# Optimization experiments

Hardware: AMD Instinct MI355X
Metric: run time of the kernel (lower is better)

Reference implementation:

```python
import jax, jax.numpy as jnp
import numpy as np

# ---------- helpers ----------

def _sqdist(a, b):
    # a: (B,n,3), b: (B,m,3) -> squared distances (B,n,m)
    return (jnp.sum(a * a, -1)[..., :, None] + jnp.sum(b * b, -1)[..., None, :]
            - 2.0 * jnp.einsum('bnd,bmd->bnm', a, b))

_gather = jax.vmap(lambda pts, idx: pts[idx])  # (N,C),(S,K)->(S,K,C) over batch


def _fps(xyz, npoint):
    # farthest point sampling; indices are non-differentiable (as in CUDA op)
    xyz = jax.lax.stop_gradient(xyz)
    B, N, _ = xyz.shape
    mind0 = jnp.sum((xyz - xyz[:, :1]) ** 2, -1)  # dist to point 0

    def step(mind, _):
        idx = jnp.argmax(mind, -1)                       # (B,)
        nxt = jnp.take_along_axis(xyz, idx[:, None, None], 1)  # (B,1,3)
        mind = jnp.minimum(mind, jnp.sum((xyz - nxt) ** 2, -1))
        return mind, idx.astype(jnp.int32)

    _, idxs = jax.lax.scan(step, mind0, None, length=npoint - 1)
    return jnp.concatenate([jnp.zeros((B, 1), jnp.int32), idxs.T], 1)  # (B,npoint)


def _ball_query(xyz, new_xyz, radius, nsample):
    # first nsample points within radius of each center, pad with first hit
    d2 = jax.lax.stop_gradient(_sqdist(new_xyz, xyz))  # (B,S,N)
    N = xyz.shape[1]
    mask = d2 < radius * radius
    key = jnp.where(mask, 0, N) + jnp.arange(N, dtype=jnp.int32)  # in-ball first, original order
    order = jnp.argsort(key, -1)
    idx = order[..., :nsample]
    cnt = mask.sum(-1, keepdims=True)
    return jnp.where(jnp.arange(nsample) < cnt, idx, idx[..., :1])


def _mlp(x, params):
    # shared MLP: 1x1 conv (+BN folded: default eval stats -> affine bias) + ReLU
    for W, b in params:
        x = jax.nn.relu(jnp.einsum('...c,co->...o', x, W) + b)
    return x


def _sa(xyz, feats, npoint, radius, nsample, params):
    # PointnetSAModuleVotes: FPS + ball-query + group(use_xyz, normalize_xyz) + MLP + max-pool
    inds = _fps(xyz, npoint)
    new_xyz = _gather(xyz, inds)                              # (B,S,3)
    idx = _ball_query(xyz, new_xyz, radius, nsample)          # (B,S,K)
    g = (_gather(xyz, idx) - new_xyz[:, :, None, :]) / radius  # normalize_xyz
    if feats is not None:
        g = jnp.concatenate([g, _gather(feats, idx)], -1)     # use_xyz: xyz first
    g = _mlp(g, params)
    return new_xyz, jnp.max(g, 2), inds                       # max over nsample


def _fp(unknown, known, feats1, feats2, params):
    # PointnetFPModule: 3-NN inverse-(squared)distance interpolation + MLP
    d2 = jax.lax.stop_gradient(_sqdist(unknown, known))       # (B,n,m)
    negd, idx = jax.lax.top_k(-d2, 3)
    d = jnp.maximum(-negd, 0.0)
    w = 1.0 / (d + 1e-8)
    w = w / jnp.sum(w, -1, keepdims=True)                     # (B,n,3)
    interp = jnp.sum(w[..., None] * _gather(feats2, idx), 2)  # (B,n,C2)
    return _mlp(jnp.concatenate([feats1, interp], -1), params)


_SPECS = {
    'sa1': [(3, 32), (32, 32), (32, 64)],
    'sa2': [(67, 64), (64, 128)],
    'sa3': [(131, 128), (128, 256)],
    'sa4': [(259, 256), (256, 256)],
    'fp1': [(512, 256), (256, 128)],
    'fp2': [(256, 128), (128, 64)],
}


def setup_inputs() -> dict:
    key = jax.random.key(0)
    ks = iter(jax.random.split(key, 64))
    inp = {'pointcloud': jax.random.uniform(next(ks), (4, 32768, 3), jnp.float32)}
    for name, dims in _SPECS.items():
        for i, (ci, co) in enumerate(dims):
            inp[f'{name}_w{i}'] = jax.random.normal(next(ks), (ci, co), jnp.float32) * 0.02
            inp[f'{name}_b{i}'] = jnp.zeros((co,), jnp.float32)
    return inp


def reference(pointcloud,
              sa1_w0, sa1_b0, sa1_w1, sa1_b1, sa1_w2, sa1_b2,
              sa2_w0, sa2_b0, sa2_w1, sa2_b1,
              sa3_w0, sa3_b0, sa3_w1, sa3_b1,
              sa4_w0, sa4_b0, sa4_w1, sa4_b1,
              fp1_w0, fp1_b0, fp1_w1, fp1_b1,
              fp2_w0, fp2_b0, fp2_w1, fp2_b1):
    P = {
        'sa1': [(sa1_w0, sa1_b0), (sa1_w1, sa1_b1), (sa1_w2, sa1_b2)],
        'sa2': [(sa2_w0, sa2_b0), (sa2_w1, sa2_b1)],
        'sa3': [(sa3_w0, sa3_b0), (sa3_w1, sa3_b1)],
        'sa4': [(sa4_w0, sa4_b0), (sa4_w1, sa4_b1)],
        'fp1': [(fp1_w0, fp1_b0), (fp1_w1, fp1_b1)],
        'fp2': [(fp2_w0, fp2_b0), (fp2_w1, fp2_b1)],
    }
    xyz = pointcloud[..., :3]  # input_feature_dim = 0 -> no extra features
    xyz1, f1, _ = _sa(xyz, None, 512, 0.1, 64, P['sa1'])
    xyz2, f2, _ = _sa(xyz1, f1, 256, 0.2, 32, P['sa2'])
    xyz3, f3, _ = _sa(xyz2, f2, 64, 0.4, 16, P['sa3'])
    xyz4, f4, _ = _sa(xyz3, f3, 16, 0.8, 16, P['sa4'])
    f = _fp(xyz3, xyz4, f3, f4, P['fp1'])   # (B,64,128)
    f = _fp(xyz2, xyz3, f2, f, P['fp2'])    # (B,256,64) == torch feats.transpose(1,2)
    return f, xyz2
```

## Files before the change

### kernel.cpp

```cpp
#include <hip/hip_runtime.h>
#include <cstddef>


__device__ __forceinline__ float sqd(float x, float y, float z, float qx, float qy, float qz) {
#pragma clang fp contract(off)
    float dx = x - qx, dy = y - qy, dz = z - qz;
    return (dx * dx + dy * dy) + dz * dz;
}

__device__ __forceinline__ float sum3sq(float x, float y, float z) {
#pragma clang fp contract(off)
    return (x * x + y * y) + z * z;
}

__device__ __forceinline__ float sqd_dot(float ax, float ay, float az, float sa_,
                                         float bx, float by, float bz) {
#pragma clang fp contract(off)
    float sb = (bx * bx + by * by) + bz * bz;
    float dt = (ax * bx + ay * by) + az * bz;
    return (sa_ + sb) - 2.0f * dt;
}

__device__ __forceinline__ unsigned long long packkey(float v, int orig) {
    return ((unsigned long long)__float_as_uint(v) << 32) | (unsigned)(~orig);
}


__global__ __launch_bounds__(512) void fps_sub(const float* __restrict__ xyz,
                                               int* __restrict__ inds,
                                               float4* __restrict__ SPall) {
    const int b = blockIdx.x, t = threadIdx.x, w = t >> 6, l = t & 63;
    const float* __restrict__ P = xyz + (size_t)b * 32768 * 3;
    float4* __restrict__ SP = SPall + (size_t)b * 32768;

    __shared__ float mind[32768];
    __shared__ int   cntS[512], offS[512], curS[512];
    __shared__ unsigned long long bkeyS[512];
    __shared__ float bxS[512], byS[512], bzS[512];
    __shared__ unsigned long long candK[8];
    __shared__ int   candB[8];
    __shared__ float bbS[6];
    __shared__ float scr[48];
    __shared__ int   qcntS;

    float mnx = 1e30f, mny = 1e30f, mnz = 1e30f;
    float mxx = -1e30f, mxy = -1e30f, mxz = -1e30f;
    for (int p = t; p < 32768; p += 512) {
        const float x = P[3 * p], y = P[3 * p + 1], z = P[3 * p + 2];
        mnx = fminf(mnx, x); mxx = fmaxf(mxx, x);
        mny = fminf(mny, y); mxy = fmaxf(mxy, y);
        mnz = fminf(mnz, z); mxz = fmaxf(mxz, z);
    }
#pragma unroll
    for (int o = 1; o < 64; o <<= 1) {
        mnx = fminf(mnx, __shfl_xor(mnx, o)); mxx = fmaxf(mxx, __shfl_xor(mxx, o));
        mny = fminf(mny, __shfl_xor(mny, o)); mxy = fmaxf(mxy, __shfl_xor(mxy, o));
        mnz = fminf(mnz, __shfl_xor(mnz, o)); mxz = fmaxf(mxz, __shfl_xor(mxz, o));
    }
    if (l == 0) {
        scr[w] = mnx; scr[8 + w] = mny; scr[16 + w] = mnz;
        scr[24 + w] = mxx; scr[32 + w] = mxy; scr[40 + w] = mxz;
    }
    __syncthreads();
    if (t == 0) {
        float a0 = 1e30f, a1 = 1e30f, a2 = 1e30f, a3 = -1e30f, a4 = -1e30f, a5 = -1e30f;
        for (int i = 0; i < 8; ++i) {
            a0 = fminf(a0, scr[i]);      a1 = fminf(a1, scr[8 + i]);
            a2 = fminf(a2, scr[16 + i]); a3 = fmaxf(a3, scr[24 + i]);
            a4 = fmaxf(a4, scr[32 + i]); a5 = fmaxf(a5, scr[40 + i]);
        }
        bbS[0] = a0; bbS[1] = a1; bbS[2] = a2; bbS[3] = a3; bbS[4] = a4; bbS[5] = a5;
        qcntS = 0;
    }
    __syncthreads();
    const float bx0 = bbS[0], by0 = bbS[1], bz0 = bbS[2];
    const float ex = bbS[3] - bx0, ey = bbS[4] - by0, ez = bbS[5] - bz0;
    const float ivx = ex > 1e-20f ? 8.0f / ex : 0.0f;
    const float ivy = ey > 1e-20f ? 8.0f / ey : 0.0f;
    const float ivz = ez > 1e-20f ? 8.0f / ez : 0.0f;

    cntS[t] = 0;
    __syncthreads();
    for (int p = t; p < 32768; p += 512) {
        const float x = P[3 * p], y = P[3 * p + 1], z = P[3 * p + 2];
        const int ix = min(7, (int)((x - bx0) * ivx));
        const int iy = min(7, (int)((y - by0) * ivy));
        const int iz = min(7, (int)((z - bz0) * ivz));
        atomicAdd(&cntS[(iz * 8 + iy) * 8 + ix], 1);
    }
    __syncthreads();

    offS[t] = cntS[t];
    __syncthreads();
    for (int d = 1; d < 512; d <<= 1) {
        const int v = (t >= d) ? offS[t - d] : 0;
        __syncthreads();
        offS[t] += v;
        __syncthreads();
    }
    const int myexc = offS[t] - cntS[t];
    offS[t] = myexc;
    curS[t] = myexc;
    __syncthreads();

    for (int p = t; p < 32768; p += 512) {
        const float x = P[3 * p], y = P[3 * p + 1], z = P[3 * p + 2];
        const int ix = min(7, (int)((x - bx0) * ivx));
        const int iy = min(7, (int)((y - by0) * ivy));
        const int iz = min(7, (int)((z - bz0) * ivz));
        const int pos = atomicAdd(&curS[(iz * 8 + iy) * 8 + ix], 1);
        SP[pos] = make_float4(x, y, z, __int_as_float(p));
    }
    for (int s = t; s < 32768; s += 512) mind[s] = 1e30f;
    const int myCnt = cntS[t];
    bkeyS[t] = (myCnt > 0) ? packkey(1e30f, 0x7fffffff) : 0ull;
    bxS[t] = 0.f; byS[t] = 0.f; bzS[t] = 0.f;
    if (t == 0) inds[b * 512] = 0;

    const int oix = t & 7, oiy = (t >> 3) & 7, oiz = t >> 6;
    const float gwx = ex * 0.125f, gwy = ey * 0.125f, gwz = ez * 0.125f;
    const float x0o = bx0 + oix * gwx, x1o = x0o + gwx;
    const float y0o = by0 + oiy * gwy, y1o = y0o + gwy;
    const float z0o = bz0 + oiz * gwz, z1o = z0o + gwz;

    const int g  = l >> 4;
    const int lg = l & 15;
    const int sg = w * 4 + g;

    float qx = P[0], qy = P[1], qz = P[2];
    __syncthreads();

    for (int k = 1; k < 512; ++k) {
        const float ddx = fmaxf(fmaxf(x0o - qx, qx - x1o), 0.0f);
        const float ddy = fmaxf(fmaxf(y0o - qy, qy - y1o), 0.0f);
        const float ddz = fmaxf(fmaxf(z0o - qz, qz - z1o), 0.0f);
        const float d2m = (ddx * ddx + ddy * ddy) + ddz * ddz;
        const float bm = __uint_as_float((unsigned)(bkeyS[t] >> 32));
        const bool act = (myCnt > 0) && (d2m <= bm * 1.0001f + 1e-9f);
        const unsigned long long pmask = __ballot(act);
        const int wcnt = __popcll(pmask);
        int wbase = 0;
        if (l == 0 && wcnt) wbase = atomicAdd(&qcntS, wcnt);
        wbase = __shfl(wbase, 0);
        if (act) curS[wbase + __popcll(pmask & ((1ull << l) - 1ull))] = t;
        __syncthreads();
        const int A = qcntS;

        for (int e = sg; e < A; e += 32) {
            const int bu = curS[e];
            const int base = offS[bu], cnt = cntS[bu];
            unsigned long long key = 0ull;
            int klane = l;
            float cx = 0.f, cy = 0.f, cz = 0.f;
            for (int c = lg; c < cnt; c += 16) {
                const float4 pt = SP[base + c];
                const float m = mind[base + c];
                const float d2 = sqd(pt.x, pt.y, pt.z, qx, qy, qz);
                const float nm = fminf(m, d2);
                mind[base + c] = nm;
                const unsigned long long kk = packkey(nm, __float_as_int(pt.w));
                if (kk > key) { key = kk; cx = pt.x; cy = pt.y; cz = pt.z; }
            }
#pragma unroll
            for (int s = 1; s < 16; s <<= 1) {
                const unsigned long long ok = __shfl_xor(key, s);
                const int ol2 = __shfl_xor(klane, s);
                if (ok > key) { key = ok; klane = ol2; }
            }
            const float wx = __shfl(cx, klane), wy = __shfl(cy, klane), wz = __shfl(cz, klane);
            if (lg == 0) {
                bkeyS[bu] = key;
                bxS[bu] = wx; byS[bu] = wy; bzS[bu] = wz;
            }
        }
        __syncthreads();

        unsigned long long key = bkeyS[t];
        int bu2 = t;
#pragma unroll
        for (int s = 1; s < 64; s <<= 1) {
            const unsigned long long ok = __shfl_xor(key, s);
            const int ob = __shfl_xor(bu2, s);
            if (ok > key) { key = ok; bu2 = ob; }
        }
        if (l == 0) { candK[w] = key; candB[w] = bu2; }
        if (t == 0) qcntS = 0;
        __syncthreads();
        unsigned long long wk = candK[0]; int wb = candB[0];
#pragma unroll
        for (int j = 1; j < 8; ++j) {
            const unsigned long long k2 = candK[j];
            if (k2 > wk) { wk = k2; wb = candB[j]; }
        }
        if (t == 0) inds[b * 512 + k] = ~(unsigned)wk;
        qx = bxS[wb]; qy = byS[wb]; qz = bzS[wb];
    }
}


template <int N, int NPOINT>
__global__ __launch_bounds__(64) void fps_small(const float* __restrict__ pts,
                                                int* __restrict__ inds) {
    constexpr int PPT = N / 64;
    const int b = blockIdx.x, l = threadIdx.x;
    const float* __restrict__ P = pts + (size_t)b * N * 3;
    float px[PPT], py[PPT], pz[PPT], md[PPT];
#pragma unroll
    for (int j = 0; j < PPT; ++j) {
        const int p = l + 64 * j;
        px[j] = P[p * 3]; py[j] = P[p * 3 + 1]; pz[j] = P[p * 3 + 2];
        md[j] = 1e30f;
    }
    float qx = P[0], qy = P[1], qz = P[2];
    if (l == 0) inds[b * NPOINT] = 0;
    for (int k = 1; k < NPOINT; ++k) {
        float bv = -1.0f;
        int   bi = 0;
#pragma unroll
        for (int j = 0; j < PPT; ++j) {
            md[j] = fminf(md[j], sqd(px[j], py[j], pz[j], qx, qy, qz));
            if (md[j] > bv) { bv = md[j]; bi = l + 64 * j; }
        }
#pragma unroll
        for (int off = 1; off < 64; off <<= 1) {
            float ov = __shfl_xor(bv, off);
            int   oi = __shfl_xor(bi, off);
            if (ov > bv || (ov == bv && oi < bi)) { bv = ov; bi = oi; }
        }
        if (l == 0) inds[b * NPOINT + k] = bi;
        const int ol = bi & 63, js = bi >> 6;
        float sx = px[0], sy = py[0], sz = pz[0];
#pragma unroll
        for (int j = 1; j < PPT; ++j) {
            if (j == js) { sx = px[j]; sy = py[j]; sz = pz[j]; }
        }
        qx = __shfl(sx, ol); qy = __shfl(sy, ol); qz = __shfl(sz, ol);
    }
}


__global__ void gather3(const float* __restrict__ src, const int* __restrict__ inds,
                        float* __restrict__ dst, int Nsrc, int M, int total) {
    const int t = blockIdx.x * 256 + threadIdx.x;
    if (t >= total) return;
    const int b = t / M;
    const int n = inds[t];
    const float* s = src + ((size_t)b * Nsrc + n) * 3;
    float* d = dst + (size_t)t * 3;
    d[0] = s[0]; d[1] = s[1]; d[2] = s[2];
}


template <int NS>
__global__ __launch_bounds__(256) void ball_query_k(const float* __restrict__ xyz,
                                                    const float* __restrict__ centers,
                                                    int* __restrict__ out,
                                                    int N, int M, float r2) {
    const int wv = blockIdx.x * 4 + (threadIdx.x >> 6);
    const int l  = threadIdx.x & 63;
    const int b  = wv / M;
    const float* cp = centers + (size_t)wv * 3;
    const float ax = cp[0], ay = cp[1], az = cp[2];
    const float sa_ = sum3sq(ax, ay, az);
    const float* __restrict__ P = xyz + (size_t)b * N * 3;
    int* o = out + (size_t)wv * NS;

    int cnt = 0, first = -1;
    float nx = P[l * 3], ny = P[l * 3 + 1], nz = P[l * 3 + 2];
    for (int i0 = 0; i0 < N; i0 += 64) {
        const float bx = nx, by = ny, bz = nz;
        if (i0 + 64 < N) {
            const int ip = (i0 + 64 + l) * 3;
            nx = P[ip]; ny = P[ip + 1]; nz = P[ip + 2];
        }
        const float d2 = sqd_dot(ax, ay, az, sa_, bx, by, bz);
        const bool in = d2 < r2;
        const unsigned long long mask = __ballot(in);
        if (first < 0 && mask != 0ull) first = i0 + __builtin_ctzll(mask);
        const int pos = cnt + __popcll(mask & ((1ull << l) - 1ull));
        if (in && pos < NS) o[pos] = i0 + l;
        cnt += __popcll(mask);
        if (cnt >= NS) break;
    }
    if (first < 0) first = 0;
    for (int p2 = cnt + l; p2 < NS; p2 += 64) o[p2] = first;
}


template <int NS, int CF, int C1, int C2, int C3>
__global__ __launch_bounds__(64) void sa_fused(
    const float* __restrict__ xyz, const float* __restrict__ feats,
    const float* __restrict__ centers, const int* __restrict__ idx,
    const float* __restrict__ w0, const float* __restrict__ b0,
    const float* __restrict__ w1, const float* __restrict__ b1,
    const float* __restrict__ w2, const float* __restrict__ b2,
    float* __restrict__ outf, int N, int M, float r) {
    constexpr int CIN = 3 + CF;
    constexpr int CL  = (C3 > 0) ? C3 : C2;
    constexpr int CPB = 64 / NS;
    const int tid = threadIdx.x;
    const int ci = tid / NS, s = tid % NS;
    const int gc = blockIdx.x * CPB + ci;
    const int b  = gc / M;
    const float* cp = centers + (size_t)gc * 3;
    const float cx = cp[0], cy = cp[1], cz = cp[2];
    const int n = idx[(size_t)gc * NS + s];
    const float* pp = xyz + ((size_t)b * N + n) * 3;
    float gi[CIN];
    gi[0] = (pp[0] - cx) / r; gi[1] = (pp[1] - cy) / r; gi[2] = (pp[2] - cz) / r;
    if constexpr (CF > 0) {
        const float* fr = feats + ((size_t)b * N + n) * CF;
#pragma unroll
        for (int c = 0; c < CF; ++c) gi[3 + c] = fr[c];
    }
    float h1[C1];
#pragma unroll
    for (int o = 0; o < C1; ++o) {
        float acc = b0[o];
#pragma unroll
        for (int k = 0; k < CIN; ++k) acc += gi[k] * w0[k * C1 + o];
        h1[o] = fmaxf(acc, 0.f);
    }
    float h2[C2];
#pragma unroll
    for (int o = 0; o < C2; ++o) {
        float acc = b1[o];
#pragma unroll
        for (int k = 0; k < C1; ++k) acc += h1[k] * w1[k * C2 + o];
        h2[o] = fmaxf(acc, 0.f);
    }
    float hl[CL];
    if constexpr (C3 > 0) {
#pragma unroll
        for (int o = 0; o < C3; ++o) {
            float acc = b2[o];
#pragma unroll
            for (int k = 0; k < C2; ++k) acc += h2[k] * w2[k * C3 + o];
            hl[o] = fmaxf(acc, 0.f);
        }
    } else {
#pragma unroll
        for (int o = 0; o < CL; ++o) hl[o] = h2[o];
    }
    __shared__ float hs[64][CL + 1];
#pragma unroll
    for (int c = 0; c < CL; ++c) hs[tid][c] = hl[c];
    __syncthreads();
    for (int cc = 0; cc < CPB; ++cc) {
        for (int c = tid; c < CL; c += 64) {
            float mx = hs[cc * NS][c];
            for (int s2 = 1; s2 < NS; ++s2) mx = fmaxf(mx, hs[cc * NS + s2][c]);
            outf[(size_t)(blockIdx.x * CPB + cc) * CL + c] = mx;
        }
    }
}


__global__ void build_g(const float* __restrict__ xyz, const float* __restrict__ feats,
                        const float* __restrict__ centers, const int* __restrict__ idx,
                        float* __restrict__ g, int N, int M, int NS, int CF, float r) {
    const int row = blockIdx.x * 4 + (threadIdx.x >> 6);
    const int l   = threadIdx.x & 63;
    const int gc  = row / NS;
    const int b   = gc / M;
    const int n   = idx[row];
    const float* cp = centers + (size_t)gc * 3;
    const float* pp = xyz + ((size_t)b * N + n) * 3;
    float* go = g + (size_t)row * (3 + CF);
    if (l < 3) go[l] = (pp[l] - cp[l]) / r;
    for (int c = l; c < CF; c += 64) go[3 + c] = feats[((size_t)b * N + n) * CF + c];
}


__global__ void dense_relu(const float* __restrict__ X, const float* __restrict__ Wm,
                           const float* __restrict__ bias, float* __restrict__ Y,
                           int M, int CI, int CO) {
    const int co = blockIdx.x * 64 + threadIdx.x;
    const int m  = blockIdx.y * 4 + threadIdx.y;
    const float* x = X + (size_t)m * CI;
    float acc = bias[co];
#pragma unroll 4
    for (int k = 0; k < CI; ++k) acc += x[k] * Wm[(size_t)k * CO + co];
    Y[(size_t)m * CO + co] = fmaxf(acc, 0.f);
}


__global__ void max_ns(const float* __restrict__ H, float* __restrict__ F,
                       int BM, int NS, int C) {
    const int tid = blockIdx.x * 256 + threadIdx.x;
    if (tid >= BM * C) return;
    const int bm = tid / C, c = tid % C;
    const float* h = H + ((size_t)bm * NS) * C + c;
    float mx = h[0];
    for (int s = 1; s < NS; ++s) mx = fmaxf(mx, h[(size_t)s * C]);
    F[tid] = mx;
}


__global__ void fp_nn(const float* __restrict__ unk, const float* __restrict__ kn,
                      int* __restrict__ nni, float* __restrict__ nnw, int NU, int NK) {
    const int t = blockIdx.x * blockDim.x + threadIdx.x;
    const int b = t / NU;
    const float* u = unk + (size_t)t * 3;
    const float ax = u[0], ay = u[1], az = u[2];
    const float sa_ = sum3sq(ax, ay, az);
    const float* K = kn + (size_t)b * NK * 3;
    float v0 = 1e30f, v1 = 1e30f, v2 = 1e30f;
    int   j0 = 0, j1 = 0, j2 = 0;
    for (int k = 0; k < NK; ++k) {
        const float d2 = sqd_dot(ax, ay, az, sa_, K[k * 3], K[k * 3 + 1], K[k * 3 + 2]);
        if (d2 < v0)      { v2 = v1; j2 = j1; v1 = v0; j1 = j0; v0 = d2; j0 = k; }
        else if (d2 < v1) { v2 = v1; j2 = j1; v1 = d2; j1 = k; }
        else if (d2 < v2) { v2 = d2; j2 = k; }
    }
    const float d0 = fmaxf(v0, 0.f), d1 = fmaxf(v1, 0.f), dd2 = fmaxf(v2, 0.f);
    float w0 = 1.f / (d0 + 1e-8f), w1 = 1.f / (d1 + 1e-8f), w2 = 1.f / (dd2 + 1e-8f);
    const float s = (w0 + w1) + w2;
    nnw[t * 3] = w0 / s; nnw[t * 3 + 1] = w1 / s; nnw[t * 3 + 2] = w2 / s;
    nni[t * 3] = j0; nni[t * 3 + 1] = j1; nni[t * 3 + 2] = j2;
}


__global__ void interp_concat(const float* __restrict__ f1, const float* __restrict__ f2,
                              const int* __restrict__ nni, const float* __restrict__ nnw,
                              float* __restrict__ X, int NU, int NK, int C1c, int C2c) {
    const int row = blockIdx.x * 4 + (threadIdx.x >> 6);
    const int l   = threadIdx.x & 63;
    const int b   = row / NU;
    const int i0 = nni[row * 3], i1 = nni[row * 3 + 1], i2 = nni[row * 3 + 2];
    const float w0 = nnw[row * 3], w1 = nnw[row * 3 + 1], w2 = nnw[row * 3 + 2];
    float* xo = X + (size_t)row * (C1c + C2c);
    for (int c = l; c < C1c; c += 64) xo[c] = f1[(size_t)row * C1c + c];
    const float* a  = f2 + ((size_t)b * NK + i0) * C2c;
    const float* bb = f2 + ((size_t)b * NK + i1) * C2c;
    const float* cc = f2 + ((size_t)b * NK + i2) * C2c;
    for (int c = l; c < C2c; c += 64) xo[C1c + c] = (w0 * a[c] + w1 * bb[c]) + w2 * cc[c];
}

__global__ void copyf(const float* __restrict__ src, float* __restrict__ dst, int n) {
    const int i = blockIdx.x * 256 + threadIdx.x;
    if (i < n) dst[i] = src[i];
}


extern "C" void kernel_launch(void* const* d_in, const int* in_sizes, int n_in,
                              void* d_out, int out_size, void* d_ws, size_t ws_size,
                              hipStream_t stream) {
    const float* xyz  = (const float*)d_in[0];
    const float* s1w0 = (const float*)d_in[1],  *s1b0 = (const float*)d_in[2];
    const float* s1w1 = (const float*)d_in[3],  *s1b1 = (const float*)d_in[4];
    const float* s1w2 = (const float*)d_in[5],  *s1b2 = (const float*)d_in[6];
    const float* s2w0 = (const float*)d_in[7],  *s2b0 = (const float*)d_in[8];
    const float* s2w1 = (const float*)d_in[9],  *s2b1 = (const float*)d_in[10];
    const float* s3w0 = (const float*)d_in[11], *s3b0 = (const float*)d_in[12];
    const float* s3w1 = (const float*)d_in[13], *s3b1 = (const float*)d_in[14];
    const float* s4w0 = (const float*)d_in[15], *s4b0 = (const float*)d_in[16];
    const float* s4w1 = (const float*)d_in[17], *s4b1 = (const float*)d_in[18];
    const float* p1w0 = (const float*)d_in[19], *p1b0 = (const float*)d_in[20];
    const float* p1w1 = (const float*)d_in[21], *p1b1 = (const float*)d_in[22];
    const float* p2w0 = (const float*)d_in[23], *p2b0 = (const float*)d_in[24];
    const float* p2w1 = (const float*)d_in[25], *p2b1 = (const float*)d_in[26];
    float* out = (float*)d_out;
    float* W = (float*)d_ws;

    size_t off = 0;
    auto A_ = [&](size_t n) { size_t o = off; off += (n + 63) & ~(size_t)63; return o; };
    const size_t o_inds1 = A_(4 * 512);
    const size_t o_xyz1  = A_(4 * 512 * 3);
    const size_t o_idx1  = A_(4 * 512 * 64);
    const size_t o_f1    = A_(4 * 512 * 64);
    const size_t o_inds2 = A_(4 * 256);
    const size_t o_xyz2  = A_(4 * 256 * 3);
    const size_t o_idx2  = A_(4 * 256 * 32);
    const size_t o_f2    = A_(4 * 256 * 128);
    const size_t o_inds3 = A_(4 * 64);
    const size_t o_xyz3  = A_(4 * 64 * 3);
    const size_t o_idx3  = A_(4 * 64 * 16);
    const size_t o_f3    = A_(4 * 64 * 256);
    const size_t o_inds4 = A_(4 * 16);
    const size_t o_xyz4  = A_(4 * 16 * 3);
    const size_t o_idx4  = A_(4 * 16 * 16);
    const size_t o_f4    = A_(4 * 16 * 256);
    const size_t o_f5    = A_(4 * 64 * 128);
    const size_t o_nni1  = A_(4 * 64 * 3);
    const size_t o_nnw1  = A_(4 * 64 * 3);
    const size_t o_nni2  = A_(4 * 256 * 3);
    const size_t o_nnw2  = A_(4 * 256 * 3);
    const size_t o_sort  = A_((size_t)4 * 32768 * 4);
    const size_t o_bufA  = A_((size_t)32768 * 128);
    const size_t o_bufB  = A_((size_t)32768 * 64);
    if (off * sizeof(float) > ws_size) return;

    int*   inds1 = (int*)(W + o_inds1); float* xyz1 = W + o_xyz1;
    int*   idx1  = (int*)(W + o_idx1);  float* f1   = W + o_f1;
    int*   inds2 = (int*)(W + o_inds2); float* xyz2 = W + o_xyz2;
    int*   idx2  = (int*)(W + o_idx2);  float* f2   = W + o_f2;
    int*   inds3 = (int*)(W + o_inds3); float* xyz3 = W + o_xyz3;
    int*   idx3  = (int*)(W + o_idx3);  float* f3   = W + o_f3;
    int*   inds4 = (int*)(W + o_inds4); float* xyz4 = W + o_xyz4;
    int*   idx4  = (int*)(W + o_idx4);  float* f4   = W + o_f4;
    float* f5    = W + o_f5;
    int*   nni1  = (int*)(W + o_nni1);  float* nnw1 = W + o_nnw1;
    int*   nni2  = (int*)(W + o_nni2);  float* nnw2 = W + o_nnw2;
    float4* sortP = (float4*)(W + o_sort);
    float* bufA  = W + o_bufA;
    float* bufB  = W + o_bufB;

    fps_sub<<<4, 512, 0, stream>>>(xyz, inds1, sortP);
    gather3<<<8, 256, 0, stream>>>(xyz, inds1, xyz1, 32768, 512, 2048);
    ball_query_k<64><<<512, 256, 0, stream>>>(xyz, xyz1, idx1, 32768, 512, (float)(0.1 * 0.1));
    sa_fused<64, 0, 32, 32, 64><<<2048, 64, 0, stream>>>(
        xyz, nullptr, xyz1, idx1, s1w0, s1b0, s1w1, s1b1, s1w2, s1b2, f1, 32768, 512, 0.1f);

    fps_small<512, 256><<<4, 64, 0, stream>>>(xyz1, inds2);
    gather3<<<4, 256, 0, stream>>>(xyz1, inds2, xyz2, 512, 256, 1024);
    ball_query_k<32><<<256, 256, 0, stream>>>(xyz1, xyz2, idx2, 512, 256, (float)(0.2 * 0.2));
    build_g<<<32768 / 4, 256, 0, stream>>>(xyz1, f1, xyz2, idx2, bufA, 512, 256, 32, 64, 0.2f);
    dense_relu<<<dim3(1, 32768 / 4), dim3(64, 4), 0, stream>>>(bufA, s2w0, s2b0, bufB, 32768, 67, 64);
    dense_relu<<<dim3(2, 32768 / 4), dim3(64, 4), 0, stream>>>(bufB, s2w1, s2b1, bufA, 32768, 64, 128);
    max_ns<<<(1024 * 128 + 255) / 256, 256, 0, stream>>>(bufA, f2, 1024, 32, 128);

    fps_small<256, 64><<<4, 64, 0, stream>>>(xyz2, inds3);
    gather3<<<1, 256, 0, stream>>>(xyz2, inds3, xyz3, 256, 64, 256);
    ball_query_k<16><<<64, 256, 0, stream>>>(xyz2, xyz3, idx3, 256, 64, (float)(0.4 * 0.4));
    build_g<<<4096 / 4, 256, 0, stream>>>(xyz2, f2, xyz3, idx3, bufA, 256, 64, 16, 128, 0.4f);
    dense_relu<<<dim3(2, 4096 / 4), dim3(64, 4), 0, stream>>>(bufA, s3w0, s3b0, bufB, 4096, 131, 128);
    dense_relu<<<dim3(4, 4096 / 4), dim3(64, 4), 0, stream>>>(bufB, s3w1, s3b1, bufA, 4096, 128, 256);
    max_ns<<<(256 * 256 + 255) / 256, 256, 0, stream>>>(bufA, f3, 256, 16, 256);

    fps_small<64, 16><<<4, 64, 0, stream>>>(xyz3, inds4);
    gather3<<<1, 256, 0, stream>>>(xyz3, inds4, xyz4, 64, 16, 64);
    ball_query_k<16><<<16, 256, 0, stream>>>(xyz3, xyz4, idx4, 64, 16, (float)(0.8 * 0.8));
    build_g<<<1024 / 4, 256, 0, stream>>>(xyz3, f3, xyz4, idx4, bufA, 64, 16, 16, 256, 0.8f);
    dense_relu<<<dim3(4, 1024 / 4), dim3(64, 4), 0, stream>>>(bufA, s4w0, s4b0, bufB, 1024, 259, 256);
    dense_relu<<<dim3(4, 1024 / 4), dim3(64, 4), 0, stream>>>(bufB, s4w1, s4b1, bufA, 1024, 256, 256);
    max_ns<<<(64 * 256 + 255) / 256, 256, 0, stream>>>(bufA, f4, 64, 16, 256);

    fp_nn<<<1, 256, 0, stream>>>(xyz3, xyz4, nni1, nnw1, 64, 16);
    interp_concat<<<256 / 4, 256, 0, stream>>>(f3, f4, nni1, nnw1, bufA, 64, 16, 256, 256);
    dense_relu<<<dim3(4, 256 / 4), dim3(64, 4), 0, stream>>>(bufA, p1w0, p1b0, bufB, 256, 512, 256);
    dense_relu<<<dim3(2, 256 / 4), dim3(64, 4), 0, stream>>>(bufB, p1w1, p1b1, f5, 256, 256, 128);

    fp_nn<<<4, 256, 0, stream>>>(xyz2, xyz3, nni2, nnw2, 256, 64);
    interp_concat<<<1024 / 4, 256, 0, stream>>>(f2, f5, nni2, nnw2, bufA, 256, 64, 128, 128);
    dense_relu<<<dim3(2, 1024 / 4), dim3(64, 4), 0, stream>>>(bufA, p2w0, p2b0, bufB, 1024, 256, 128);
    dense_relu<<<dim3(1, 1024 / 4), dim3(64, 4), 0, stream>>>(bufB, p2w1, p2b1, out, 1024, 128, 64);

    copyf<<<12, 256, 0, stream>>>(xyz2, out + 65536, 3072);
}
```

Before: 2.218 ms.

## Use dense full-scan FPS for early iterations before switching to bucket pruning

For the first iterations of farthest point sampling, when almost every grid bucket would pass the pruning test anyway, each wave now scans its contiguous slab of sorted points directly with unrolled loads. This skips the ballot, compaction and per-bucket reduction overhead. At iteration K_DENSE every bucket is forced active so the per-bucket max keys are rebuilt before pruning resumes. Launch bounds also request two blocks per CU. The risk is that the dense path does extra distance work if pruning would already have been effective early on.

New measurement: 2.431 ms. 1.1x slower.

```diff
diff --git a/kernel.cpp b/kernel.cpp
--- a/kernel.cpp
+++ b/kernel.cpp
@@ -26,9 +26,11 @@
 }
 
 
-__global__ __launch_bounds__(512) void fps_sub(const float* __restrict__ xyz,
-                                               int* __restrict__ inds,
-                                               float4* __restrict__ SPall) {
+#define K_DENSE 40
+
+__global__ __launch_bounds__(512, 2) void fps_sub(const float* __restrict__ xyz,
+                                                  int* __restrict__ inds,
+                                                  float4* __restrict__ SPall) {
     const int b = blockIdx.x, t = threadIdx.x, w = t >> 6, l = t & 63;
     const float* __restrict__ P = xyz + (size_t)b * 32768 * 3;
     float4* __restrict__ SP = SPall + (size_t)b * 32768;
@@ -126,74 +128,111 @@
     const int g  = l >> 4;
     const int lg = l & 15;
     const int sg = w * 4 + g;
+    const int wslab = w * 4096;
 
     float qx = P[0], qy = P[1], qz = P[2];
     __syncthreads();
 
     for (int k = 1; k < 512; ++k) {
-        const float ddx = fmaxf(fmaxf(x0o - qx, qx - x1o), 0.0f);
-        const float ddy = fmaxf(fmaxf(y0o - qy, qy - y1o), 0.0f);
-        const float ddz = fmaxf(fmaxf(z0o - qz, qz - z1o), 0.0f);
-        const float d2m = (ddx * ddx + ddy * ddy) + ddz * ddz;
-        const float bm = __uint_as_float((unsigned)(bkeyS[t] >> 32));
-        const bool act = (myCnt > 0) && (d2m <= bm * 1.0001f + 1e-9f);
-        const unsigned long long pmask = __ballot(act);
-        const int wcnt = __popcll(pmask);
-        int wbase = 0;
-        if (l == 0 && wcnt) wbase = atomicAdd(&qcntS, wcnt);
-        wbase = __shfl(wbase, 0);
-        if (act) curS[wbase + __popcll(pmask & ((1ull << l) - 1ull))] = t;
-        __syncthreads();
-        const int A = qcntS;
-
-        for (int e = sg; e < A; e += 32) {
-            const int bu = curS[e];
-            const int base = offS[bu], cnt = cntS[bu];
+        if (k < K_DENSE) {
             unsigned long long key = 0ull;
-            int klane = l;
-            float cx = 0.f, cy = 0.f, cz = 0.f;
-            for (int c = lg; c < cnt; c += 16) {
-                const float4 pt = SP[base + c];
-                const float m = mind[base + c];
-                const float d2 = sqd(pt.x, pt.y, pt.z, qx, qy, qz);
-                const float nm = fminf(m, d2);
-                mind[base + c] = nm;
-                const unsigned long long kk = packkey(nm, __float_as_int(pt.w));
-                if (kk > key) { key = kk; cx = pt.x; cy = pt.y; cz = pt.z; }
+            for (int r0 = 0; r0 < 64; r0 += 8) {
+                float4 pt[8]; float mm[8];
+                const int i0 = wslab + r0 * 64 + l;
+#pragma unroll
+                for (int u = 0; u < 8; ++u) pt[u] = SP[i0 + u * 64];
+#pragma unroll
+                for (int u = 0; u < 8; ++u) mm[u] = mind[i0 + u * 64];
+#pragma unroll
+                for (int u = 0; u < 8; ++u) {
+                    const float d2 = sqd(pt[u].x, pt[u].y, pt[u].z, qx, qy, qz);
+                    const float nm = fminf(mm[u], d2);
+                    mind[i0 + u * 64] = nm;
+                    const unsigned long long kk = packkey(nm, __float_as_int(pt[u].w));
+                    if (kk > key) key = kk;
+                }
             }
 #pragma unroll
-            for (int s = 1; s < 16; s <<= 1) {
+            for (int s = 1; s < 64; s <<= 1) {
                 const unsigned long long ok = __shfl_xor(key, s);
-                const int ol2 = __shfl_xor(klane, s);
-                if (ok > key) { key = ok; klane = ol2; }
+                if (ok > key) key = ok;
             }
-            const float wx = __shfl(cx, klane), wy = __shfl(cy, klane), wz = __shfl(cz, klane);
-            if (lg == 0) {
-                bkeyS[bu] = key;
-                bxS[bu] = wx; byS[bu] = wy; bzS[bu] = wz;
+            if (l == 0) candK[w] = key;
+            __syncthreads();
+            unsigned long long wk = candK[0];
+#pragma unroll
+            for (int j = 1; j < 8; ++j) if (candK[j] > wk) wk = candK[j];
+            const int worig = (int)~(unsigned)wk;
+            if (t == 0) inds[b * 512 + k] = worig;
+            const float* qp = P + 3 * (size_t)worig;
+            qx = qp[0]; qy = qp[1]; qz = qp[2];
+            __syncthreads();
+        } else {
+            const float ddx = fmaxf(fmaxf(x0o - qx, qx - x1o), 0.0f);
+            const float ddy = fmaxf(fmaxf(y0o - qy, qy - y1o), 0.0f);
+            const float ddz = fmaxf(fmaxf(z0o - qz, qz - z1o), 0.0f);
+            const float d2m = (ddx * ddx + ddy * ddy) + ddz * ddz;
+            const float bm = __uint_as_float((unsigned)(bkeyS[t] >> 32));
+            const bool act = (myCnt > 0) &&
+                             (k == K_DENSE || d2m <= bm * 1.0001f + 1e-9f);
+            const unsigned long long pmask = __ballot(act);
+            const int wcnt = __popcll(pmask);
+            int wbase = 0;
+            if (l == 0 && wcnt) wbase = atomicAdd(&qcntS, wcnt);
+            wbase = __shfl(wbase, 0);
+            if (act) curS[wbase + __popcll(pmask & ((1ull << l) - 1ull))] = t;
+            __syncthreads();
+            const int A = qcntS;
+
+            for (int e = sg; e < A; e += 32) {
+                const int bu = curS[e];
+                const int base = offS[bu], cnt = cntS[bu];
+                unsigned long long key = 0ull;
+                int klane = l;
+                float cx = 0.f, cy = 0.f, cz = 0.f;
+                for (int c = lg; c < cnt; c += 16) {
+                    const float4 pt = SP[base + c];
+                    const float m = mind[base + c];
+                    const float d2 = sqd(pt.x, pt.y, pt.z, qx, qy, qz);
+                    const float nm = fminf(m, d2);
+                    mind[base + c] = nm;
+                    const unsigned long long kk = packkey(nm, __float_as_int(pt.w));
+                    if (kk > key) { key = kk; cx = pt.x; cy = pt.y; cz = pt.z; }
+                }
+#pragma unroll
+                for (int s = 1; s < 16; s <<= 1) {
+                    const unsigned long long ok = __shfl_xor(key, s);
+                    const int ol2 = __shfl_xor(klane, s);
+                    if (ok > key) { key = ok; klane = ol2; }
+                }
+                const float wx = __shfl(cx, klane), wy = __shfl(cy, klane), wz = __shfl(cz, klane);
+                if (lg == 0) {
+                    bkeyS[bu] = key;
+                    bxS[bu] = wx; byS[bu] = wy; bzS[bu] = wz;
+                }
             }
-        }
-        __syncthreads();
-
-        unsigned long long key = bkeyS[t];
-        int bu2 = t;
-#pragma unroll
-        for (int s = 1; s < 64; s <<= 1) {
-            const unsigned long long ok = __shfl_xor(key, s);
-            const int ob = __shfl_xor(bu2, s);
-            if (ok > key) { key = ok; bu2 = ob; }
-        }
-        if (l == 0) { candK[w] = key; candB[w] = bu2; }
-        if (t == 0) qcntS = 0;
-        __syncthreads();
-        unsigned long long wk = candK[0]; int wb = candB[0];
-#pragma unroll
-        for (int j = 1; j < 8; ++j) {
-            const unsigned long long k2 = candK[j];
-            if (k2 > wk) { wk = k2; wb = candB[j]; }
-        }
-        if (t == 0) inds[b * 512 + k] = ~(unsigned)wk;
-        qx = bxS[wb]; qy = byS[wb]; qz = bzS[wb];
+            __syncthreads();
+
+            unsigned long long key = bkeyS[t];
+            int bu2 = t;
+#pragma unroll
+            for (int s = 1; s < 64; s <<= 1) {
+                const unsigned long long ok = __shfl_xor(key, s);
+                const int ob = __shfl_xor(bu2, s);
+                if (ok > key) { key = ok; bu2 = ob; }
+            }
+            if (l == 0) { candK[w] = key; candB[w] = bu2; }
+            if (t == 0) qcntS = 0;
+            __syncthreads();
+            unsigned long long wk = candK[0]; int wb = candB[0];
+#pragma unroll
+            for (int j = 1; j < 8; ++j) {
+                const unsigned long long k2 = candK[j];
+                if (k2 > wk) { wk = k2; wb = candB[j]; }
+            }
+            if (t == 0) inds[b * 512 + k] = (int)~(unsigned)wk;
+            qx = bxS[wb]; qy = byS[wb]; qz = bzS[wb];
+        }
     }
 }
 
```

## Fuse gathers, ball query, grouping, max-pool and FP interpolation into neighbouring kernels

Applied to the files above, without the earlier changes.

FPS kernels now write the sampled coordinates directly, which removes the separate gather3 launches. Ball query is fused with the SA1 MLP and, in the later stages, with group building, so neighbour indices stay in shared memory. The last dense layer of each SA stage is fused with max-pooling, and FP interpolation is fused into the first dense layer. This cuts launch count and intermediate global traffic, but dense_relu_max and dense_fp recompute per-row loads with less parallelism per block.

Measured after the change: 2.457 ms. 10.8% more time.

```diff
diff --git a/kernel.cpp b/kernel.cpp
--- a/kernel.cpp
+++ b/kernel.cpp
@@ -28,7 +28,8 @@
 
 __global__ __launch_bounds__(512) void fps_sub(const float* __restrict__ xyz,
                                                int* __restrict__ inds,
-                                               float4* __restrict__ SPall) {
+                                               float4* __restrict__ SPall,
+                                               float* __restrict__ gout) {
     const int b = blockIdx.x, t = threadIdx.x, w = t >> 6, l = t & 63;
     const float* __restrict__ P = xyz + (size_t)b * 32768 * 3;
     float4* __restrict__ SP = SPall + (size_t)b * 32768;
@@ -115,7 +116,12 @@
     const int myCnt = cntS[t];
     bkeyS[t] = (myCnt > 0) ? packkey(1e30f, 0x7fffffff) : 0ull;
     bxS[t] = 0.f; byS[t] = 0.f; bzS[t] = 0.f;
-    if (t == 0) inds[b * 512] = 0;
+    if (t == 0) {
+        inds[b * 512] = 0;
+        gout[(size_t)b * 512 * 3 + 0] = P[0];
+        gout[(size_t)b * 512 * 3 + 1] = P[1];
+        gout[(size_t)b * 512 * 3 + 2] = P[2];
+    }
 
     const int oix = t & 7, oiy = (t >> 3) & 7, oiz = t >> 6;
     const float gwx = ex * 0.125f, gwy = ey * 0.125f, gwz = ez * 0.125f;
@@ -192,15 +198,20 @@
             const unsigned long long k2 = candK[j];
             if (k2 > wk) { wk = k2; wb = candB[j]; }
         }
-        if (t == 0) inds[b * 512 + k] = ~(unsigned)wk;
         qx = bxS[wb]; qy = byS[wb]; qz = bzS[wb];
+        if (t == 0) {
+            inds[b * 512 + k] = (int)~(unsigned)wk;
+            gout[((size_t)b * 512 + k) * 3 + 0] = qx;
+            gout[((size_t)b * 512 + k) * 3 + 1] = qy;
+            gout[((size_t)b * 512 + k) * 3 + 2] = qz;
+        }
     }
 }
 
 
 template <int N, int NPOINT>
 __global__ __launch_bounds__(64) void fps_small(const float* __restrict__ pts,
-                                                int* __restrict__ inds) {
+                                                float* __restrict__ gout) {
     constexpr int PPT = N / 64;
     const int b = blockIdx.x, l = threadIdx.x;
     const float* __restrict__ P = pts + (size_t)b * N * 3;
@@ -212,7 +223,11 @@
         md[j] = 1e30f;
     }
     float qx = P[0], qy = P[1], qz = P[2];
-    if (l == 0) inds[b * NPOINT] = 0;
+    if (l == 0) {
+        gout[(size_t)b * NPOINT * 3 + 0] = qx;
+        gout[(size_t)b * NPOINT * 3 + 1] = qy;
+        gout[(size_t)b * NPOINT * 3 + 2] = qz;
+    }
     for (int k = 1; k < NPOINT; ++k) {
         float bv = -1.0f;
         int   bi = 0;
@@ -227,7 +242,6 @@
             int   oi = __shfl_xor(bi, off);
             if (ov > bv || (ov == bv && oi < bi)) { bv = ov; bi = oi; }
         }
-        if (l == 0) inds[b * NPOINT + k] = bi;
         const int ol = bi & 63, js = bi >> 6;
         float sx = px[0], sy = py[0], sz = pz[0];
 #pragma unroll
@@ -235,35 +249,101 @@
             if (j == js) { sx = px[j]; sy = py[j]; sz = pz[j]; }
         }
         qx = __shfl(sx, ol); qy = __shfl(sy, ol); qz = __shfl(sz, ol);
-    }
-}
-
-
-__global__ void gather3(const float* __restrict__ src, const int* __restrict__ inds,
-                        float* __restrict__ dst, int Nsrc, int M, int total) {
-    const int t = blockIdx.x * 256 + threadIdx.x;
-    if (t >= total) return;
-    const int b = t / M;
-    const int n = inds[t];
-    const float* s = src + ((size_t)b * Nsrc + n) * 3;
-    float* d = dst + (size_t)t * 3;
-    d[0] = s[0]; d[1] = s[1]; d[2] = s[2];
+        if (l == 0) {
+            gout[((size_t)b * NPOINT + k) * 3 + 0] = qx;
+            gout[((size_t)b * NPOINT + k) * 3 + 1] = qy;
+            gout[((size_t)b * NPOINT + k) * 3 + 2] = qz;
+        }
+    }
+}
+
+
+__global__ __launch_bounds__(64) void sa1_fused(
+    const float* __restrict__ xyz, const float* __restrict__ centers,
+    const float* __restrict__ w0, const float* __restrict__ b0,
+    const float* __restrict__ w1, const float* __restrict__ b1,
+    const float* __restrict__ w2, const float* __restrict__ b2,
+    float* __restrict__ outf, float r2, float r) {
+    const int gc = blockIdx.x;
+    const int b  = gc >> 9;
+    const int l  = threadIdx.x;
+    const float* __restrict__ P = xyz + (size_t)b * 32768 * 3;
+    const float* cp = centers + (size_t)gc * 3;
+    const float cx = cp[0], cy = cp[1], cz = cp[2];
+    const float sa_ = sum3sq(cx, cy, cz);
+    __shared__ int idxS[64];
+
+    int cnt = 0, first = -1;
+    float nx = P[l * 3], ny = P[l * 3 + 1], nz = P[l * 3 + 2];
+    for (int i0 = 0; i0 < 32768; i0 += 64) {
+        const float bx = nx, by = ny, bz = nz;
+        if (i0 + 64 < 32768) {
+            const int ip = (i0 + 64 + l) * 3;
+            nx = P[ip]; ny = P[ip + 1]; nz = P[ip + 2];
+        }
+        const float d2 = sqd_dot(cx, cy, cz, sa_, bx, by, bz);
+        const bool in = d2 < r2;
+        const unsigned long long mask = __ballot(in);
+        if (first < 0 && mask != 0ull) first = i0 + __builtin_ctzll(mask);
+        const int pos = cnt + __popcll(mask & ((1ull << l) - 1ull));
+        if (in && pos < 64) idxS[pos] = i0 + l;
+        cnt += __popcll(mask);
+        if (cnt >= 64) break;
+    }
+    if (first < 0) first = 0;
+    for (int p2 = cnt + l; p2 < 64; p2 += 64) idxS[p2] = first;
+    __syncthreads();
+
+    const int n = idxS[l];
+    const float* pp = P + (size_t)n * 3;
+    float gi[3];
+    gi[0] = (pp[0] - cx) / r; gi[1] = (pp[1] - cy) / r; gi[2] = (pp[2] - cz) / r;
+    float h1[32];
+#pragma unroll
+    for (int o = 0; o < 32; ++o) {
+        float acc = b0[o];
+#pragma unroll
+        for (int k = 0; k < 3; ++k) acc += gi[k] * w0[k * 32 + o];
+        h1[o] = fmaxf(acc, 0.f);
+    }
+    float h2[32];
+#pragma unroll
+    for (int o = 0; o < 32; ++o) {
+        float acc = b1[o];
+#pragma unroll
+        for (int k = 0; k < 32; ++k) acc += h1[k] * w1[k * 32 + o];
+        h2[o] = fmaxf(acc, 0.f);
+    }
+    __shared__ float hs[64][65];
+#pragma unroll
+    for (int o = 0; o < 64; ++o) {
+        float acc = b2[o];
+#pragma unroll
+        for (int k = 0; k < 32; ++k) acc += h2[k] * w2[k * 64 + o];
+        hs[l][o] = fmaxf(acc, 0.f);
+    }
+    __syncthreads();
+    float mx = hs[0][l];
+    for (int s2 = 1; s2 < 64; ++s2) mx = fmaxf(mx, hs[s2][l]);
+    outf[(size_t)gc * 64 + l] = mx;
 }
 
 
 template <int NS>
-__global__ __launch_bounds__(256) void ball_query_k(const float* __restrict__ xyz,
-                                                    const float* __restrict__ centers,
-                                                    int* __restrict__ out,
-                                                    int N, int M, float r2) {
+__global__ __launch_bounds__(256) void bqb(const float* __restrict__ xyz_src,
+                                           const float* __restrict__ centers,
+                                           const float* __restrict__ feats,
+                                           float* __restrict__ g,
+                                           int N, int M, int CF, float r, float r2) {
     const int wv = blockIdx.x * 4 + (threadIdx.x >> 6);
+    const int w  = threadIdx.x >> 6;
     const int l  = threadIdx.x & 63;
     const int b  = wv / M;
+    __shared__ int idxS[4][NS];
     const float* cp = centers + (size_t)wv * 3;
     const float ax = cp[0], ay = cp[1], az = cp[2];
     const float sa_ = sum3sq(ax, ay, az);
-    const float* __restrict__ P = xyz + (size_t)b * N * 3;
-    int* o = out + (size_t)wv * NS;
+    const float* __restrict__ P = xyz_src + (size_t)b * N * 3;
 
     int cnt = 0, first = -1;
     float nx = P[l * 3], ny = P[l * 3 + 1], nz = P[l * 3 + 2];
@@ -278,97 +358,21 @@
         const unsigned long long mask = __ballot(in);
         if (first < 0 && mask != 0ull) first = i0 + __builtin_ctzll(mask);
         const int pos = cnt + __popcll(mask & ((1ull << l) - 1ull));
-        if (in && pos < NS) o[pos] = i0 + l;
+        if (in && pos < NS) idxS[w][pos] = i0 + l;
         cnt += __popcll(mask);
         if (cnt >= NS) break;
     }
     if (first < 0) first = 0;
-    for (int p2 = cnt + l; p2 < NS; p2 += 64) o[p2] = first;
-}
-
-
-template <int NS, int CF, int C1, int C2, int C3>
-__global__ __launch_bounds__(64) void sa_fused(
-    const float* __restrict__ xyz, const float* __restrict__ feats,
-    const float* __restrict__ centers, const int* __restrict__ idx,
-    const float* __restrict__ w0, const float* __restrict__ b0,
-    const float* __restrict__ w1, const float* __restrict__ b1,
-    const float* __restrict__ w2, const float* __restrict__ b2,
-    float* __restrict__ outf, int N, int M, float r) {
-    constexpr int CIN = 3 + CF;
-    constexpr int CL  = (C3 > 0) ? C3 : C2;
-    constexpr int CPB = 64 / NS;
-    const int tid = threadIdx.x;
-    const int ci = tid / NS, s = tid % NS;
-    const int gc = blockIdx.x * CPB + ci;
-    const int b  = gc / M;
-    const float* cp = centers + (size_t)gc * 3;
-    const float cx = cp[0], cy = cp[1], cz = cp[2];
-    const int n = idx[(size_t)gc * NS + s];
-    const float* pp = xyz + ((size_t)b * N + n) * 3;
-    float gi[CIN];
-    gi[0] = (pp[0] - cx) / r; gi[1] = (pp[1] - cy) / r; gi[2] = (pp[2] - cz) / r;
-    if constexpr (CF > 0) {
-        const float* fr = feats + ((size_t)b * N + n) * CF;
-#pragma unroll
-        for (int c = 0; c < CF; ++c) gi[3 + c] = fr[c];
-    }
-    float h1[C1];
-#pragma unroll
-    for (int o = 0; o < C1; ++o) {
-        float acc = b0[o];
-#pragma unroll
-        for (int k = 0; k < CIN; ++k) acc += gi[k] * w0[k * C1 + o];
-        h1[o] = fmaxf(acc, 0.f);
-    }
-    float h2[C2];
-#pragma unroll
-    for (int o = 0; o < C2; ++o) {
-        float acc = b1[o];
-#pragma unroll
-        for (int k = 0; k < C1; ++k) acc += h1[k] * w1[k * C2 + o];
-        h2[o] = fmaxf(acc, 0.f);
-    }
-    float hl[CL];
-    if constexpr (C3 > 0) {
-#pragma unroll
-        for (int o = 0; o < C3; ++o) {
-            float acc = b2[o];
-#pragma unroll
-            for (int k = 0; k < C2; ++k) acc += h2[k] * w2[k * C3 + o];
-            hl[o] = fmaxf(acc, 0.f);
-        }
-    } else {
-#pragma unroll
-        for (int o = 0; o < CL; ++o) hl[o] = h2[o];
-    }
-    __shared__ float hs[64][CL + 1];
-#pragma unroll
-    for (int c = 0; c < CL; ++c) hs[tid][c] = hl[c];
-    __syncthreads();
-    for (int cc = 0; cc < CPB; ++cc) {
-        for (int c = tid; c < CL; c += 64) {
-            float mx = hs[cc * NS][c];
-            for (int s2 = 1; s2 < NS; ++s2) mx = fmaxf(mx, hs[cc * NS + s2][c]);
-            outf[(size_t)(blockIdx.x * CPB + cc) * CL + c] = mx;
-        }
-    }
-}
-
-
-__global__ void build_g(const float* __restrict__ xyz, const float* __restrict__ feats,
-                        const float* __restrict__ centers, const int* __restrict__ idx,
-                        float* __restrict__ g, int N, int M, int NS, int CF, float r) {
-    const int row = blockIdx.x * 4 + (threadIdx.x >> 6);
-    const int l   = threadIdx.x & 63;
-    const int gc  = row / NS;
-    const int b   = gc / M;
-    const int n   = idx[row];
-    const float* cp = centers + (size_t)gc * 3;
-    const float* pp = xyz + ((size_t)b * N + n) * 3;
-    float* go = g + (size_t)row * (3 + CF);
-    if (l < 3) go[l] = (pp[l] - cp[l]) / r;
-    for (int c = l; c < CF; c += 64) go[3 + c] = feats[((size_t)b * N + n) * CF + c];
+    for (int p2 = cnt + l; p2 < NS; p2 += 64) idxS[w][p2] = first;
+    __syncthreads();
+
+    for (int s = 0; s < NS; ++s) {
+        const int n = idxS[w][s];
+        float* go = g + ((size_t)wv * NS + s) * (3 + CF);
+        const float* pp = P + (size_t)n * 3;
+        if (l < 3) go[l] = (pp[l] - cp[l]) / r;
+        for (int c = l; c < CF; c += 64) go[3 + c] = feats[((size_t)b * N + n) * CF + c];
+    }
 }
 
 
@@ -385,15 +389,21 @@
 }
 
 
-__global__ void max_ns(const float* __restrict__ H, float* __restrict__ F,
-                       int BM, int NS, int C) {
-    const int tid = blockIdx.x * 256 + threadIdx.x;
-    if (tid >= BM * C) return;
-    const int bm = tid / C, c = tid % C;
-    const float* h = H + ((size_t)bm * NS) * C + c;
-    float mx = h[0];
-    for (int s = 1; s < NS; ++s) mx = fmaxf(mx, h[(size_t)s * C]);
-    F[tid] = mx;
+__global__ void dense_relu_max(const float* __restrict__ X, const float* __restrict__ Wm,
+                               const float* __restrict__ bias, float* __restrict__ F,
+                               int NS, int CI, int CO) {
+    const int co = blockIdx.x * 64 + threadIdx.x;
+    const int bm = blockIdx.y;
+    const float b0 = bias[co];
+    float mx = -1e30f;
+    for (int s = 0; s < NS; ++s) {
+        const float* x = X + ((size_t)bm * NS + s) * CI;
+        float acc = b0;
+#pragma unroll 4
+        for (int k = 0; k < CI; ++k) acc += x[k] * Wm[(size_t)k * CO + co];
+        mx = fmaxf(mx, fmaxf(acc, 0.f));
+    }
+    F[(size_t)bm * CO + co] = mx;
 }
 
 
@@ -421,20 +431,28 @@
 }
 
 
-__global__ void interp_concat(const float* __restrict__ f1, const float* __restrict__ f2,
-                              const int* __restrict__ nni, const float* __restrict__ nnw,
-                              float* __restrict__ X, int NU, int NK, int C1c, int C2c) {
-    const int row = blockIdx.x * 4 + (threadIdx.x >> 6);
-    const int l   = threadIdx.x & 63;
-    const int b   = row / NU;
-    const int i0 = nni[row * 3], i1 = nni[row * 3 + 1], i2 = nni[row * 3 + 2];
-    const float w0 = nnw[row * 3], w1 = nnw[row * 3 + 1], w2 = nnw[row * 3 + 2];
-    float* xo = X + (size_t)row * (C1c + C2c);
-    for (int c = l; c < C1c; c += 64) xo[c] = f1[(size_t)row * C1c + c];
-    const float* a  = f2 + ((size_t)b * NK + i0) * C2c;
-    const float* bb = f2 + ((size_t)b * NK + i1) * C2c;
-    const float* cc = f2 + ((size_t)b * NK + i2) * C2c;
-    for (int c = l; c < C2c; c += 64) xo[C1c + c] = (w0 * a[c] + w1 * bb[c]) + w2 * cc[c];
+__global__ void dense_fp(const float* __restrict__ f1c, const float* __restrict__ f2c,
+                         const int* __restrict__ nni, const float* __restrict__ nnw,
+                         const float* __restrict__ Wm, const float* __restrict__ bias,
+                         float* __restrict__ Y, int NU, int NK, int C1c, int C2c, int CO) {
+    const int co = blockIdx.x * 64 + threadIdx.x;
+    const int m  = blockIdx.y * 4 + threadIdx.y;
+    const int b  = m / NU;
+    const int i0 = nni[m * 3], i1 = nni[m * 3 + 1], i2 = nni[m * 3 + 2];
+    const float w0 = nnw[m * 3], w1 = nnw[m * 3 + 1], w2 = nnw[m * 3 + 2];
+    const float* x1 = f1c + (size_t)m * C1c;
+    const float* a  = f2c + ((size_t)b * NK + i0) * C2c;
+    const float* bb = f2c + ((size_t)b * NK + i1) * C2c;
+    const float* cc = f2c + ((size_t)b * NK + i2) * C2c;
+    float acc = bias[co];
+#pragma unroll 4
+    for (int k = 0; k < C1c; ++k) acc += x1[k] * Wm[(size_t)k * CO + co];
+#pragma unroll 4
+    for (int k = 0; k < C2c; ++k) {
+        const float xi = (w0 * a[k] + w1 * bb[k]) + w2 * cc[k];
+        acc += xi * Wm[(size_t)(C1c + k) * CO + co];
+    }
+    Y[(size_t)m * CO + co] = fmaxf(acc, 0.f);
 }
 
 __global__ void copyf(const float* __restrict__ src, float* __restrict__ dst, int n) {
@@ -467,19 +485,12 @@
     auto A_ = [&](size_t n) { size_t o = off; off += (n + 63) & ~(size_t)63; return o; };
     const size_t o_inds1 = A_(4 * 512);
     const size_t o_xyz1  = A_(4 * 512 * 3);
-    const size_t o_idx1  = A_(4 * 512 * 64);
     const size_t o_f1    = A_(4 * 512 * 64);
-    const size_t o_inds2 = A_(4 * 256);
     const size_t o_xyz2  = A_(4 * 256 * 3);
-    const size_t o_idx2  = A_(4 * 256 * 32);
     const size_t o_f2    = A_(4 * 256 * 128);
-    const size_t o_inds3 = A_(4 * 64);
     const size_t o_xyz3  = A_(4 * 64 * 3);
-    const size_t o_idx3  = A_(4 * 64 * 16);
     const size_t o_f3    = A_(4 * 64 * 256);
-    const size_t o_inds4 = A_(4 * 16);
     const size_t o_xyz4  = A_(4 * 16 * 3);
-    const size_t o_idx4  = A_(4 * 16 * 16);
     const size_t o_f4    = A_(4 * 16 * 256);
     const size_t o_f5    = A_(4 * 64 * 128);
     const size_t o_nni1  = A_(4 * 64 * 3);
@@ -492,13 +503,10 @@
     if (off * sizeof(float) > ws_size) return;
 
     int*   inds1 = (int*)(W + o_inds1); float* xyz1 = W + o_xyz1;
-    int*   idx1  = (int*)(W + o_idx1);  float* f1   = W + o_f1;
-    int*   inds2 = (int*)(W + o_inds2); float* xyz2 = W + o_xyz2;
-    int*   idx2  = (int*)(W + o_idx2);  float* f2   = W + o_f2;
-    int*   inds3 = (int*)(W + o_inds3); float* xyz3 = W + o_xyz3;
-    int*   idx3  = (int*)(W + o_idx3);  float* f3   = W + o_f3;
-    int*   inds4 = (int*)(W + o_inds4); float* xyz4 = W + o_xyz4;
-    int*   idx4  = (int*)(W + o_idx4);  float* f4   = W + o_f4;
+    float* f1    = W + o_f1;
+    float* xyz2  = W + o_xyz2;          float* f2   = W + o_f2;
+    float* xyz3  = W + o_xyz3;          float* f3   = W + o_f3;
+    float* xyz4  = W + o_xyz4;          float* f4   = W + o_f4;
     float* f5    = W + o_f5;
     int*   nni1  = (int*)(W + o_nni1);  float* nnw1 = W + o_nnw1;
     int*   nni2  = (int*)(W + o_nni2);  float* nnw2 = W + o_nnw2;
@@ -506,45 +514,37 @@
     float* bufA  = W + o_bufA;
     float* bufB  = W + o_bufB;
 
-    fps_sub<<<4, 512, 0, stream>>>(xyz, inds1, sortP);
-    gather3<<<8, 256, 0, stream>>>(xyz, inds1, xyz1, 32768, 512, 2048);
-    ball_query_k<64><<<512, 256, 0, stream>>>(xyz, xyz1, idx1, 32768, 512, (float)(0.1 * 0.1));
-    sa_fused<64, 0, 32, 32, 64><<<2048, 64, 0, stream>>>(
-        xyz, nullptr, xyz1, idx1, s1w0, s1b0, s1w1, s1b1, s1w2, s1b2, f1, 32768, 512, 0.1f);
-
-    fps_small<512, 256><<<4, 64, 0, stream>>>(xyz1, inds2);
-    gather3<<<4, 256, 0, stream>>>(xyz1, inds2, xyz2, 512, 256, 1024);
-    ball_query_k<32><<<256, 256, 0, stream>>>(xyz1, xyz2, idx2, 512, 256, (float)(0.2 * 0.2));
-    build_g<<<32768 / 4, 256, 0, stream>>>(xyz1, f1, xyz2, idx2, bufA, 512, 256, 32, 64, 0.2f);
-    dense_relu<<<dim3(1, 32768 / 4), dim3(64, 4), 0, stream>>>(bufA, s2w0, s2b0, bufB, 32768, 67, 64);
-    dense_relu<<<dim3(2, 32768 / 4), dim3(64, 4), 0, stream>>>(bufB, s2w1, s2b1, bufA, 32768, 64, 128);
-    max_ns<<<(1024 * 128 + 255) / 256, 256, 0, stream>>>(bufA, f2, 1024, 32, 128);
-
-    fps_small<256, 64><<<4, 64, 0, stream>>>(xyz2, inds3);
-    gather3<<<1, 256, 0, stream>>>(xyz2, inds3, xyz3, 256, 64, 256);
-    ball_query_k<16><<<64, 256, 0, stream>>>(xyz2, xyz3, idx3, 256, 64, (float)(0.4 * 0.4));
-    build_g<<<4096 / 4, 256, 0, stream>>>(xyz2, f2, xyz3, idx3, bufA, 256, 64, 16, 128, 0.4f);
-    dense_relu<<<dim3(2, 4096 / 4), dim3(64, 4), 0, stream>>>(bufA, s3w0, s3b0, bufB, 4096, 131, 128);
-    dense_relu<<<dim3(4, 4096 / 4), dim3(64, 4), 0, stream>>>(bufB, s3w1, s3b1, bufA, 4096, 128, 256);
-    max_ns<<<(256 * 256 + 255) / 256, 256, 0, stream>>>(bufA, f3, 256, 16, 256);
-
-    fps_small<64, 16><<<4, 64, 0, stream>>>(xyz3, inds4);
-    gather3<<<1, 256, 0, stream>>>(xyz3, inds4, xyz4, 64, 16, 64);
-    ball_query_k<16><<<16, 256, 0, stream>>>(xyz3, xyz4, idx4, 64, 16, (float)(0.8 * 0.8));
-    build_g<<<1024 / 4, 256, 0, stream>>>(xyz3, f3, xyz4, idx4, bufA, 64, 16, 16, 256, 0.8f);
-    dense_relu<<<dim3(4, 1024 / 4), dim3(64, 4), 0, stream>>>(bufA, s4w0, s4b0, bufB, 1024, 259, 256);
-    dense_relu<<<dim3(4, 1024 / 4), dim3(64, 4), 0, stream>>>(bufB, s4w1, s4b1, bufA, 1024, 256, 256);
-    max_ns<<<(64 * 256 + 255) / 256, 256, 0, stream>>>(bufA, f4, 64, 16, 256);
+    fps_sub<<<4, 512, 0, stream>>>(xyz, inds1, sortP, xyz1);
+    sa1_fused<<<2048, 64, 0, stream>>>(xyz, xyz1, s1w0, s1b0, s1w1, s1b1, s1w2, s1b2,
+                                       f1, (float)(0.1 * 0.1), 0.1f);
+
+    fps_small<512, 256><<<4, 64, 0, stream>>>(xyz1, xyz2);
+    bqb<32><<<256, 256, 0, stream>>>(xyz1, xyz2, f1, bufA, 512, 256, 64, 0.2f,
+                                     (float)(0.2 * 0.2));
+    dense_relu<<<dim3(1, 8192), dim3(64, 4), 0, stream>>>(bufA, s2w0, s2b0, bufB, 32768, 67, 64);
+    dense_relu_max<<<dim3(2, 1024), 64, 0, stream>>>(bufB, s2w1, s2b1, f2, 32, 64, 128);
+
+    fps_small<256, 64><<<4, 64, 0, stream>>>(xyz2, xyz3);
+    bqb<16><<<64, 256, 0, stream>>>(xyz2, xyz3, f2, bufA, 256, 64, 128, 0.4f,
+                                    (float)(0.4 * 0.4));
+    dense_relu<<<dim3(2, 1024), dim3(64, 4), 0, stream>>>(bufA, s3w0, s3b0, bufB, 4096, 131, 128);
+    dense_relu_max<<<dim3(4, 256), 64, 0, stream>>>(bufB, s3w1, s3b1, f3, 16, 128, 256);
+
+    fps_small<64, 16><<<4, 64, 0, stream>>>(xyz3, xyz4);
+    bqb<16><<<16, 256, 0, stream>>>(xyz3, xyz4, f3, bufA, 64, 16, 256, 0.8f,
+                                    (float)(0.8 * 0.8));
+    dense_relu<<<dim3(4, 256), dim3(64, 4), 0, stream>>>(bufA, s4w0, s4b0, bufB, 1024, 259, 256);
+    dense_relu_max<<<dim3(4, 64), 64, 0, stream>>>(bufB, s4w1, s4b1, f4, 16, 256, 256);
 
     fp_nn<<<1, 256, 0, stream>>>(xyz3, xyz4, nni1, nnw1, 64, 16);
-    interp_concat<<<256 / 4, 256, 0, stream>>>(f3, f4, nni1, nnw1, bufA, 64, 16, 256, 256);
-    dense_relu<<<dim3(4, 256 / 4), dim3(64, 4), 0, stream>>>(bufA, p1w0, p1b0, bufB, 256, 512, 256);
-    dense_relu<<<dim3(2, 256 / 4), dim3(64, 4), 0, stream>>>(bufB, p1w1, p1b1, f5, 256, 256, 128);
+    dense_fp<<<dim3(4, 64), dim3(64, 4), 0, stream>>>(f3, f4, nni1, nnw1, p1w0, p1b0,
+                                                      bufB, 64, 16, 256, 256, 256);
+    dense_relu<<<dim3(2, 64), dim3(64, 4), 0, stream>>>(bufB, p1w1, p1b1, f5, 256, 256, 128);
 
     fp_nn<<<4, 256, 0, stream>>>(xyz2, xyz3, nni2, nnw2, 256, 64);
-    interp_concat<<<1024 / 4, 256, 0, stream>>>(f2, f5, nni2, nnw2, bufA, 256, 64, 128, 128);
-    dense_relu<<<dim3(2, 1024 / 4), dim3(64, 4), 0, stream>>>(bufA, p2w0, p2b0, bufB, 1024, 256, 128);
-    dense_relu<<<dim3(1, 1024 / 4), dim3(64, 4), 0, stream>>>(bufB, p2w1, p2b1, out, 1024, 128, 64);
+    dense_fp<<<dim3(2, 256), dim3(64, 4), 0, stream>>>(f2, f5, nni2, nnw2, p2w0, p2b0,
+                                                       bufB, 256, 64, 128, 128, 128);
+    dense_relu<<<dim3(1, 256), dim3(64, 4), 0, stream>>>(bufB, p2w1, p2b1, out, 1024, 128, 64);
 
     copyf<<<12, 256, 0, stream>>>(xyz2, out + 65536, 3072);
 }
```
